# Kernel optimization log

Hardware: AMD Instinct MI355X
Metric: run time of the kernel (lower is better)

Reference implementation:

```python
import jax, jax.numpy as jnp
import numpy as np

N_NODES = 20000
BN_EPS = 1e-5


def setup_inputs() -> dict:
    key = jax.random.key(0)
    ks = jax.random.split(key, 8)
    in_dim, half, out_dim, n_edges = 256, 128, 256, 320000
    s = 1.0 / np.sqrt(in_dim)
    return {
        "x": jax.random.normal(ks[0], (N_NODES, in_dim), dtype=jnp.float32),
        "edge_index": jax.random.randint(ks[1], (2, n_edges), 0, N_NODES, dtype=jnp.int64),
        "W_l_f": jax.random.normal(ks[2], (half, in_dim), dtype=jnp.float32) * s,
        "b_l_f": jnp.zeros((half,), dtype=jnp.float32),
        "W_r_f": jax.random.normal(ks[3], (half, in_dim), dtype=jnp.float32) * s,
        "W_l_b": jax.random.normal(ks[4], (half, in_dim), dtype=jnp.float32) * s,
        "b_l_b": jnp.zeros((half,), dtype=jnp.float32),
        "W_r_b": jax.random.normal(ks[5], (half, in_dim), dtype=jnp.float32) * s,
        "gamma": jnp.ones((out_dim,), dtype=jnp.float32),
        "beta": jnp.zeros((out_dim,), dtype=jnp.float32),
    }


def _sage(x, src, dst, W_l, b_l, W_r):
    # mean-aggregate source features at destination nodes (PyG SAGEConv, aggr='mean')
    msg_sum = jax.ops.segment_sum(x[src], dst, num_segments=N_NODES)
    cnt = jax.ops.segment_sum(jnp.ones((src.shape[0],), x.dtype), dst, num_segments=N_NODES)
    aggr = msg_sum / jnp.maximum(cnt, 1.0)[:, None]
    # lin_l(aggr) + lin_r(x); lin_l carries the bias in PyG
    return aggr @ W_l.T + b_l + x @ W_r.T


def reference(x, edge_index, W_l_f, b_l_f, W_r_f, W_l_b, b_l_b, W_r_b, gamma, beta):
    src, dst = edge_index[0], edge_index[1]
    h_fwd = _sage(x, src, dst, W_l_f, b_l_f, W_r_f)
    h_bwd = _sage(x, dst, src, W_l_b, b_l_b, W_r_b)  # flipped edges
    h = jnp.concatenate([h_fwd, h_bwd], axis=-1)  # [N, out_dim]
    # BatchNorm1d in training mode (N > 1), biased variance
    mean = jnp.mean(h, axis=0)
    var = jnp.mean(jnp.square(h - mean), axis=0)
    h = (h - mean) * jax.lax.rsqrt(var + BN_EPS) * gamma + beta
    return jax.nn.relu(h)
```

## Files before the change

### kernel.cpp

```cpp
#include <hip/hip_runtime.h>
#include <hip/hip_bf16.h>

#define N_NODES 20000
#define N_EDGES 320000
#define BN_EPS  1e-5f

typedef __attribute__((ext_vector_type(4))) float f32x4;
typedef __attribute__((ext_vector_type(8))) __bf16 bf16x8;
typedef __attribute__((ext_vector_type(4))) unsigned short u16x4;

__device__ __forceinline__ unsigned short f2bf(float f) {
    unsigned int u = __float_as_uint(f);
    u += 0x7fffu + ((u >> 16) & 1u);
    return (unsigned short)(u >> 16);
}
__device__ __forceinline__ float bflo(unsigned int u) { return __uint_as_float(u << 16); }
__device__ __forceinline__ float bfhi(unsigned int u) { return __uint_as_float(u & 0xffff0000u); }

__device__ __forceinline__ void gload_lds16(const void* g, void* l) {
    __builtin_amdgcn_global_load_lds(
        (const __attribute__((address_space(1))) void*)g,
        (__attribute__((address_space(3))) void*)l, 16, 0, 0);
}

__global__ void count_kernel(const int* __restrict__ src, const int* __restrict__ dst,
                             int* __restrict__ cntF, int* __restrict__ cntB) {
    int e = blockIdx.x * blockDim.x + threadIdx.x;
    if (e < N_EDGES) {
        atomicAdd(&cntF[dst[e]], 1);
        atomicAdd(&cntB[src[e]], 1);
    }
}

#define SCAN_PER 20
__global__ __launch_bounds__(1024) void scan_kernel(const int* __restrict__ cntF, int* __restrict__ offF,
                                                    const int* __restrict__ cntB, int* __restrict__ offB) {
    const int* in  = blockIdx.x ? cntB : cntF;
    int*       out = blockIdx.x ? offB : offF;
    int t = threadIdx.x;
    int base = t * SCAN_PER;
    int v[SCAN_PER];
    int sum = 0;
    #pragma unroll
    for (int k = 0; k < SCAN_PER; ++k) {
        int i = base + k;
        int c = (i < N_NODES) ? in[i] : 0;
        v[k] = sum; sum += c;
    }
    __shared__ int sh[1024];
    sh[t] = sum;
    __syncthreads();
    for (int o = 1; o < 1024; o <<= 1) {
        int x = (t >= o) ? sh[t - o] : 0;
        __syncthreads();
        sh[t] += x;
        __syncthreads();
    }
    int pre = t ? sh[t - 1] : 0;
    #pragma unroll
    for (int k = 0; k < SCAN_PER; ++k) {
        int i = base + k;
        if (i < N_NODES) out[i] = pre + v[k];
    }
    if (t == 1023) out[N_NODES] = sh[1023];
}

__global__ void fill_kernel(const int* __restrict__ src, const int* __restrict__ dst,
                            const int* __restrict__ offF, const int* __restrict__ offB,
                            int* __restrict__ curF, int* __restrict__ curB,
                            int* __restrict__ listF, int* __restrict__ listB) {
    int e = blockIdx.x * blockDim.x + threadIdx.x;
    if (e < N_EDGES) {
        int s = src[e], d = dst[e];
        int p = atomicAdd(&curF[d], 1);
        listF[offF[d] + p] = s;
        int q = atomicAdd(&curB[s], 1);
        listB[offB[s] + q] = d;
    }
}

__global__ __launch_bounds__(256) void cvt_kernel(
    const float* __restrict__ x,
    const float* __restrict__ Wlf, const float* __restrict__ Wlb,
    const float* __restrict__ Wrf, const float* __restrict__ Wrb,
    unsigned short* __restrict__ Xb, unsigned short* __restrict__ Wb)
{
    const int XQ = N_NODES * 256 / 4;
    const int WQ = 128 * 256 / 4;
    const int total = XQ + 4 * WQ;
    for (int i = blockIdx.x * blockDim.x + threadIdx.x; i < total; i += gridDim.x * blockDim.x) {
        const float* sp;
        unsigned short* dp;
        if (i < XQ) {
            sp = x + (size_t)i * 4;
            dp = Xb + (size_t)i * 4;
        } else {
            int w = i - XQ;
            int mat = w / WQ;
            int o = (w - mat * WQ) * 4;
            if      (mat == 0) sp = Wlf + o;
            else if (mat == 1) sp = Wlb + o;
            else if (mat == 2) sp = Wrf + o;
            else               sp = Wrb + o;
            dp = Wb + (size_t)mat * 32768 + o;
        }
        float4 v = *(const float4*)sp;
        u16x4 r = {f2bf(v.x), f2bf(v.y), f2bf(v.z), f2bf(v.w)};
        *(u16x4*)dp = r;
    }
}

__global__ __launch_bounds__(256) void mfma_gemm_kernel(
    const unsigned short* __restrict__ Xb, const unsigned short* __restrict__ Wb,
    unsigned short* __restrict__ Y, float* __restrict__ Z)
{
    __shared__ unsigned short As[128 * 64];
    __shared__ unsigned short Bs[128 * 64];
    int by = blockIdx.y;
    int mBase = blockIdx.x * 128;
    int tid = threadIdx.x, lane = tid & 63, wave = tid >> 6;
    int wr = wave >> 1, wc = wave & 1;
    const unsigned short* W = Wb + (size_t)by * 128 * 256;

    f32x4 acc[4][4] = {};

    for (int k0 = 0; k0 < 256; k0 += 64) {
        #pragma unroll
        for (int c = 0; c < 4; ++c) {
            int S = c * 256 + tid;
            int row = S >> 3;
            int q = (S & 7) ^ (row & 7);
            int gm = mBase + row; gm = gm < N_NODES ? gm : N_NODES - 1;
            gload_lds16(Xb + (size_t)gm * 256 + k0 + q * 8, &As[S * 8]);
            gload_lds16(W + (size_t)row * 256 + k0 + q * 8, &Bs[S * 8]);
        }
        asm volatile("s_waitcnt vmcnt(0)" ::: "memory");
        __syncthreads();

        #pragma unroll
        for (int ks = 0; ks < 2; ++ks) {
            bf16x8 af[4], bfr[4];
            int sl = ks * 4 + (lane >> 4);
            #pragma unroll
            for (int m = 0; m < 4; ++m) {
                int row = wr * 64 + m * 16 + (lane & 15);
                af[m] = *(const bf16x8*)&As[row * 64 + ((sl ^ (row & 7)) * 8)];
            }
            #pragma unroll
            for (int n = 0; n < 4; ++n) {
                int row = wc * 64 + n * 16 + (lane & 15);
                bfr[n] = *(const bf16x8*)&Bs[row * 64 + ((sl ^ (row & 7)) * 8)];
            }
            #pragma unroll
            for (int m = 0; m < 4; ++m)
                #pragma unroll
                for (int n = 0; n < 4; ++n)
                    acc[m][n] = __builtin_amdgcn_mfma_f32_16x16x32_bf16(af[m], bfr[n], acc[m][n], 0, 0, 0);
        }
        __syncthreads();
    }

    bool toY = by < 2;
    int cBase = (by & 1) * 128 + wc * 64;
    #pragma unroll
    for (int m = 0; m < 4; ++m) {
        int gm0 = mBase + wr * 64 + m * 16 + (lane >> 4) * 4;
        #pragma unroll
        for (int n = 0; n < 4; ++n) {
            int gn = cBase + n * 16 + (lane & 15);
            f32x4 v = acc[m][n];
            #pragma unroll
            for (int j = 0; j < 4; ++j) {
                int gm = gm0 + j;
                if (gm < N_NODES) {
                    if (toY) Y[(size_t)gm * 256 + gn] = f2bf(v[j]);
                    else     Z[(size_t)gm * 256 + gn] = v[j];
                }
            }
        }
    }
}

#define NPW 2
__global__ __launch_bounds__(256) void aggregate_kernel(
    const unsigned short* __restrict__ Y,
    const int* __restrict__ offF, const int* __restrict__ listF,
    const int* __restrict__ offB, const int* __restrict__ listB,
    float* __restrict__ H)
{
    int tid = threadIdx.x, lane = tid & 63, wave = tid >> 6;
    int dir = wave >> 1, half = wave & 1;
    const int* off  = dir ? offB : offF;
    const int* list = dir ? listB : listF;
    int eg = lane >> 4;
    int c16 = lane & 15;
    int nodeBase = blockIdx.x * (2 * NPW) + half * NPW;

    for (int jn = 0; jn < NPW; ++jn) {
        int n = nodeBase + jn;
        int beg = off[n], end = off[n + 1];
        int deg = end - beg;
        float acc[8] = {0.f, 0.f, 0.f, 0.f, 0.f, 0.f, 0.f, 0.f};

        for (int i = beg; i < end; i += 64) {
            int c = end - i; if (c > 64) c = 64;
            int u_l = list[i + (lane < c ? lane : c - 1)];
            int nb = (c + 15) >> 4;
            for (int b = 0; b < nb; ++b) {
                uint4 v[4]; float mk[4];
                #pragma unroll
                for (int k = 0; k < 4; ++k) {
                    int ei = b * 16 + k * 4 + eg;
                    mk[k] = (ei < c) ? 1.f : 0.f;
                    int u = __shfl(u_l, ei < c ? ei : c - 1);
                    v[k] = *(const uint4*)(Y + (size_t)u * 256 + dir * 128 + c16 * 8);
                }
                #pragma unroll
                for (int k = 0; k < 4; ++k) {
                    acc[0] = fmaf(mk[k], bflo(v[k].x), acc[0]);
                    acc[1] = fmaf(mk[k], bfhi(v[k].x), acc[1]);
                    acc[2] = fmaf(mk[k], bflo(v[k].y), acc[2]);
                    acc[3] = fmaf(mk[k], bfhi(v[k].y), acc[3]);
                    acc[4] = fmaf(mk[k], bflo(v[k].z), acc[4]);
                    acc[5] = fmaf(mk[k], bfhi(v[k].z), acc[5]);
                    acc[6] = fmaf(mk[k], bflo(v[k].w), acc[6]);
                    acc[7] = fmaf(mk[k], bfhi(v[k].w), acc[7]);
                }
            }
        }
        #pragma unroll
        for (int j = 0; j < 8; ++j) {
            acc[j] += __shfl_xor(acc[j], 16);
            acc[j] += __shfl_xor(acc[j], 32);
        }
        float h0 = (eg & 2) ? ((eg & 1) ? acc[6] : acc[4]) : ((eg & 1) ? acc[2] : acc[0]);
        float h1 = (eg & 2) ? ((eg & 1) ? acc[7] : acc[5]) : ((eg & 1) ? acc[3] : acc[1]);
        float inv = 1.f / fmaxf((float)deg, 1.f);
        float2* hp = (float2*)(H + (size_t)n * 256 + dir * 128 + c16 * 8 + eg * 2);
        float2 z = *hp;
        *hp = make_float2(fmaf(h0, inv, z.x), fmaf(h1, inv, z.y));
    }
}

__global__ __launch_bounds__(256) void bn_stats_kernel(const float* __restrict__ H,
                                                       float* __restrict__ stats) {
    int col = threadIdx.x;
    float s1 = 0.f, s2 = 0.f;
    for (int n = blockIdx.x; n < N_NODES; n += gridDim.x) {
        float h = H[(size_t)n * 256 + col];
        s1 += h;
        s2 += h * h;
    }
    atomicAdd(&stats[col], s1);
    atomicAdd(&stats[256 + col], s2);
}

__global__ __launch_bounds__(256) void bn_kernel(
    const float* __restrict__ stats, const float* __restrict__ gamma,
    const float* __restrict__ beta, float* __restrict__ H)
{
    __shared__ float sc[256], sf[256];
    int tid = threadIdx.x;
    {
        float mean = stats[tid] * (1.f / N_NODES);
        float var  = stats[256 + tid] * (1.f / N_NODES) - mean * mean;
        float s = rsqrtf(fmaxf(var, 0.f) + BN_EPS) * gamma[tid];
        sc[tid] = s;
        sf[tid] = beta[tid] - mean * s;
    }
    __syncthreads();
    for (int n = blockIdx.x; n < N_NODES; n += gridDim.x) {
        size_t idx = (size_t)n * 256 + tid;
        float h = H[idx];
        H[idx] = fmaxf(h * sc[tid] + sf[tid], 0.f);
    }
}

extern "C" void kernel_launch(void* const* d_in, const int* in_sizes, int n_in,
                              void* d_out, int out_size, void* d_ws, size_t ws_size,
                              hipStream_t stream) {
    const float* x     = (const float*)d_in[0];
    const int*   edge  = (const int*)d_in[1];
    const float* Wlf   = (const float*)d_in[2];
    const float* Wrf   = (const float*)d_in[4];
    const float* Wlb   = (const float*)d_in[5];
    const float* Wrb   = (const float*)d_in[7];
    const float* gamma = (const float*)d_in[8];
    const float* beta  = (const float*)d_in[9];
    float* out = (float*)d_out;

    const int* src = edge;
    const int* dst = edge + N_EDGES;

    char* ws = (char*)d_ws;
    size_t off = 0;
    auto alloc = [&](size_t bytes) { size_t r = off; off += (bytes + 255) & ~(size_t)255; return r; };
    unsigned short* Y  = (unsigned short*)(ws + alloc((size_t)N_NODES * 256 * 2));
    unsigned short* Xb = (unsigned short*)(ws + alloc((size_t)N_NODES * 256 * 2));
    unsigned short* Wb = (unsigned short*)(ws + alloc((size_t)4 * 128 * 256 * 2));
    int* offF  = (int*)(ws + alloc((size_t)(N_NODES + 1) * 4));
    int* offB  = (int*)(ws + alloc((size_t)(N_NODES + 1) * 4));
    int* listF = (int*)(ws + alloc((size_t)N_EDGES * 4));
    int* listB = (int*)(ws + alloc((size_t)N_EDGES * 4));
    size_t zbase_off = off;
    int* cntF = (int*)(ws + alloc((size_t)N_NODES * 4));
    int* cntB = (int*)(ws + alloc((size_t)N_NODES * 4));
    int* curF = (int*)(ws + alloc((size_t)N_NODES * 4));
    int* curB = (int*)(ws + alloc((size_t)N_NODES * 4));
    float* stats = (float*)(ws + alloc(512 * 4));
    size_t zbytes = off - zbase_off;

    hipMemsetAsync(ws + zbase_off, 0, zbytes, stream);

    cvt_kernel<<<2048, 256, 0, stream>>>(x, Wlf, Wlb, Wrf, Wrb, Xb, Wb);

    count_kernel<<<(N_EDGES + 255) / 256, 256, 0, stream>>>(src, dst, cntF, cntB);
    scan_kernel<<<2, 1024, 0, stream>>>(cntF, offF, cntB, offB);
    fill_kernel<<<(N_EDGES + 255) / 256, 256, 0, stream>>>(src, dst, offF, offB, curF, curB, listF, listB);

    dim3 ggrid((N_NODES + 127) / 128, 4);
    mfma_gemm_kernel<<<ggrid, 256, 0, stream>>>(Xb, Wb, Y, out);

    aggregate_kernel<<<N_NODES / (2 * NPW), 256, 0, stream>>>(
        Y, offF, listF, offB, listB, out);

    bn_stats_kernel<<<512, 256, 0, stream>>>(out, stats);
    bn_kernel<<<2048, 256, 0, stream>>>(stats, gamma, beta, out);
}
```

Before: 159.0 us.

## Fold memset into convert kernel, merge fill with GEMM, predicate aggregate loads

The workspace memset is folded into the bf16 conversion kernel, removing a separate memset launch. The CSR fill kernel and the MFMA GEMM are merged into one launch with block-index dispatch, so independent fill blocks and GEMM tiles can run concurrently. In aggregation, out-of-range neighbor loads are skipped by predication instead of being loaded and masked with FMAs. Risks are a heavier kernel that mixes atomic fill work with LDS-heavy GEMM blocks, and an added tail loop for zeroing.

```diff
diff --git a/kernel.cpp b/kernel.cpp
--- a/kernel.cpp
+++ b/kernel.cpp
@@ -4,6 +4,9 @@
 #define N_NODES 20000
 #define N_EDGES 320000
 #define BN_EPS  1e-5f
+
+#define FILL_BLK ((N_EDGES + 255) / 256)
+#define GEMM_MT  ((N_NODES + 127) / 128)
 
 typedef __attribute__((ext_vector_type(4))) float f32x4;
 typedef __attribute__((ext_vector_type(8))) __bf16 bf16x8;
@@ -21,6 +24,42 @@
     __builtin_amdgcn_global_load_lds(
         (const __attribute__((address_space(1))) void*)g,
         (__attribute__((address_space(3))) void*)l, 16, 0, 0);
+}
+
+__global__ __launch_bounds__(256) void cvt_zero_kernel(
+    const float* __restrict__ x,
+    const float* __restrict__ Wlf, const float* __restrict__ Wlb,
+    const float* __restrict__ Wrf, const float* __restrict__ Wrb,
+    unsigned short* __restrict__ Xb, unsigned short* __restrict__ Wb,
+    uint4* __restrict__ zp, int zquads)
+{
+    const int XQ = N_NODES * 256 / 4;
+    const int WQ = 128 * 256 / 4;
+    const int total = XQ + 4 * WQ + zquads;
+    for (int i = blockIdx.x * blockDim.x + threadIdx.x; i < total; i += gridDim.x * blockDim.x) {
+        if (i >= XQ + 4 * WQ) {
+            zp[i - XQ - 4 * WQ] = make_uint4(0, 0, 0, 0);
+            continue;
+        }
+        const float* sp;
+        unsigned short* dp;
+        if (i < XQ) {
+            sp = x + (size_t)i * 4;
+            dp = Xb + (size_t)i * 4;
+        } else {
+            int w = i - XQ;
+            int mat = w / WQ;
+            int o = (w - mat * WQ) * 4;
+            if      (mat == 0) sp = Wlf + o;
+            else if (mat == 1) sp = Wlb + o;
+            else if (mat == 2) sp = Wrf + o;
+            else               sp = Wrb + o;
+            dp = Wb + (size_t)mat * 32768 + o;
+        }
+        float4 v = *(const float4*)sp;
+        u16x4 r = {f2bf(v.x), f2bf(v.y), f2bf(v.z), f2bf(v.w)};
+        *(u16x4*)dp = r;
+    }
 }
 
 __global__ void count_kernel(const int* __restrict__ src, const int* __restrict__ dst,
@@ -65,59 +104,32 @@
     if (t == 1023) out[N_NODES] = sh[1023];
 }
 
-__global__ void fill_kernel(const int* __restrict__ src, const int* __restrict__ dst,
-                            const int* __restrict__ offF, const int* __restrict__ offB,
-                            int* __restrict__ curF, int* __restrict__ curB,
-                            int* __restrict__ listF, int* __restrict__ listB) {
-    int e = blockIdx.x * blockDim.x + threadIdx.x;
-    if (e < N_EDGES) {
-        int s = src[e], d = dst[e];
-        int p = atomicAdd(&curF[d], 1);
-        listF[offF[d] + p] = s;
-        int q = atomicAdd(&curB[s], 1);
-        listB[offB[s] + q] = d;
-    }
-}
-
-__global__ __launch_bounds__(256) void cvt_kernel(
-    const float* __restrict__ x,
-    const float* __restrict__ Wlf, const float* __restrict__ Wlb,
-    const float* __restrict__ Wrf, const float* __restrict__ Wrb,
-    unsigned short* __restrict__ Xb, unsigned short* __restrict__ Wb)
-{
-    const int XQ = N_NODES * 256 / 4;
-    const int WQ = 128 * 256 / 4;
-    const int total = XQ + 4 * WQ;
-    for (int i = blockIdx.x * blockDim.x + threadIdx.x; i < total; i += gridDim.x * blockDim.x) {
-        const float* sp;
-        unsigned short* dp;
-        if (i < XQ) {
-            sp = x + (size_t)i * 4;
-            dp = Xb + (size_t)i * 4;
-        } else {
-            int w = i - XQ;
-            int mat = w / WQ;
-            int o = (w - mat * WQ) * 4;
-            if      (mat == 0) sp = Wlf + o;
-            else if (mat == 1) sp = Wlb + o;
-            else if (mat == 2) sp = Wrf + o;
-            else               sp = Wrb + o;
-            dp = Wb + (size_t)mat * 32768 + o;
-        }
-        float4 v = *(const float4*)sp;
-        u16x4 r = {f2bf(v.x), f2bf(v.y), f2bf(v.z), f2bf(v.w)};
-        *(u16x4*)dp = r;
-    }
-}
-
-__global__ __launch_bounds__(256) void mfma_gemm_kernel(
+__global__ __launch_bounds__(256) void fill_gemm_kernel(
+    const int* __restrict__ src, const int* __restrict__ dst,
+    const int* __restrict__ offF, const int* __restrict__ offB,
+    int* __restrict__ curF, int* __restrict__ curB,
+    int* __restrict__ listF, int* __restrict__ listB,
     const unsigned short* __restrict__ Xb, const unsigned short* __restrict__ Wb,
     unsigned short* __restrict__ Y, float* __restrict__ Z)
 {
     __shared__ unsigned short As[128 * 64];
     __shared__ unsigned short Bs[128 * 64];
-    int by = blockIdx.y;
-    int mBase = blockIdx.x * 128;
+
+    if (blockIdx.x < FILL_BLK) {
+        int e = blockIdx.x * blockDim.x + threadIdx.x;
+        if (e < N_EDGES) {
+            int s = src[e], d = dst[e];
+            int p = atomicAdd(&curF[d], 1);
+            listF[offF[d] + p] = s;
+            int q = atomicAdd(&curB[s], 1);
+            listB[offB[s] + q] = d;
+        }
+        return;
+    }
+
+    int gb = blockIdx.x - FILL_BLK;
+    int by = gb & 3;
+    int mBase = (gb >> 2) * 128;
     int tid = threadIdx.x, lane = tid & 63, wave = tid >> 6;
     int wr = wave >> 1, wc = wave & 1;
     const unsigned short* W = Wb + (size_t)by * 128 * 256;
@@ -204,27 +216,23 @@
 
         for (int i = beg; i < end; i += 64) {
             int c = end - i; if (c > 64) c = 64;
-            int u_l = list[i + (lane < c ? lane : c - 1)];
-            int nb = (c + 15) >> 4;
-            for (int b = 0; b < nb; ++b) {
-                uint4 v[4]; float mk[4];
+            int u_l = list[i + (lane < c ? lane : 0)];
+            for (int e0 = 0; e0 < c; e0 += 16) {
+                uint4 v[4];
                 #pragma unroll
                 for (int k = 0; k < 4; ++k) {
-                    int ei = b * 16 + k * 4 + eg;
-                    mk[k] = (ei < c) ? 1.f : 0.f;
-                    int u = __shfl(u_l, ei < c ? ei : c - 1);
-                    v[k] = *(const uint4*)(Y + (size_t)u * 256 + dir * 128 + c16 * 8);
+                    int ei = e0 + k * 4 + eg;
+                    int u = __shfl(u_l, ei < c ? ei : 0);
+                    v[k] = make_uint4(0u, 0u, 0u, 0u);
+                    if (ei < c)
+                        v[k] = *(const uint4*)(Y + (size_t)u * 256 + dir * 128 + c16 * 8);
                 }
                 #pragma unroll
                 for (int k = 0; k < 4; ++k) {
-                    acc[0] = fmaf(mk[k], bflo(v[k].x), acc[0]);
-                    acc[1] = fmaf(mk[k], bfhi(v[k].x), acc[1]);
-                    acc[2] = fmaf(mk[k], bflo(v[k].y), acc[2]);
-                    acc[3] = fmaf(mk[k], bfhi(v[k].y), acc[3]);
-                    acc[4] = fmaf(mk[k], bflo(v[k].z), acc[4]);
-                    acc[5] = fmaf(mk[k], bfhi(v[k].z), acc[5]);
-                    acc[6] = fmaf(mk[k], bflo(v[k].w), acc[6]);
-                    acc[7] = fmaf(mk[k], bfhi(v[k].w), acc[7]);
+                    acc[0] += bflo(v[k].x); acc[1] += bfhi(v[k].x);
+                    acc[2] += bflo(v[k].y); acc[3] += bfhi(v[k].y);
+                    acc[4] += bflo(v[k].z); acc[5] += bfhi(v[k].z);
+                    acc[6] += bflo(v[k].w); acc[7] += bfhi(v[k].w);
                 }
             }
         }
@@ -310,16 +318,14 @@
     float* stats = (float*)(ws + alloc(512 * 4));
     size_t zbytes = off - zbase_off;
 
-    hipMemsetAsync(ws + zbase_off, 0, zbytes, stream);
-
-    cvt_kernel<<<2048, 256, 0, stream>>>(x, Wlf, Wlb, Wrf, Wrb, Xb, Wb);
-
-    count_kernel<<<(N_EDGES + 255) / 256, 256, 0, stream>>>(src, dst, cntF, cntB);
+    cvt_zero_kernel<<<2048, 256, 0, stream>>>(x, Wlf, Wlb, Wrf, Wrb, Xb, Wb,
+                                              (uint4*)(ws + zbase_off), (int)(zbytes / 16));
+
+    count_kernel<<<FILL_BLK, 256, 0, stream>>>(src, dst, cntF, cntB);
     scan_kernel<<<2, 1024, 0, stream>>>(cntF, offF, cntB, offB);
-    fill_kernel<<<(N_EDGES + 255) / 256, 256, 0, stream>>>(src, dst, offF, offB, curF, curB, listF, listB);
-
-    dim3 ggrid((N_NODES + 127) / 128, 4);
-    mfma_gemm_kernel<<<ggrid, 256, 0, stream>>>(Xb, Wb, Y, out);
+
+    fill_gemm_kernel<<<FILL_BLK + GEMM_MT * 4, 256, 0, stream>>>(
+        src, dst, offF, offB, curF, curB, listF, listB, Xb, Wb, Y, out);
 
     aggregate_kernel<<<N_NODES / (2 * NPW), 256, 0, stream>>>(
         Y, offF, listF, offB, listB, out);
```

New measurement: 150.9 us. 5.1% less time.
